# Performance work log

Hardware: AMD Instinct MI355X
Metric: run time of the kernel (lower is better)

Reference implementation:

```python
import jax, jax.numpy as jnp
import numpy as np

HIDDEN = 1024
BATCH = 4
SEQ = 4096
KQ = 4096  # number of query positions ('k' in the docstring)


def setup_inputs() -> dict:
    key = jax.random.key(0)
    ks = jax.random.split(key, 9)
    s = 1.0 / np.sqrt(HIDDEN)
    return {
        "queries": jax.random.normal(ks[0], (BATCH, KQ, HIDDEN), jnp.float32),
        "keys": jax.random.normal(ks[1], (BATCH, SEQ, HIDDEN), jnp.float32),
        "values": jax.random.normal(ks[2], (BATCH, SEQ, HIDDEN), jnp.float32),
        # nn.Linear params: y = x @ W.T + b
        "Wq": jax.random.normal(ks[3], (HIDDEN, HIDDEN), jnp.float32) * s,
        "bq": jax.random.normal(ks[4], (HIDDEN,), jnp.float32) * s,
        "Wk": jax.random.normal(ks[5], (HIDDEN, HIDDEN), jnp.float32) * s,
        "bk": jax.random.normal(ks[6], (HIDDEN,), jnp.float32) * s,
        "Wv": jax.random.normal(ks[7], (HIDDEN, HIDDEN), jnp.float32) * s,
        "bv": jax.random.normal(ks[8], (HIDDEN,), jnp.float32) * s,
    }


def reference(queries, keys, values, Wq, bq, Wk, bk, Wv, bv):
    hidden = keys.shape[-1]
    scaling = jax.lax.rsqrt(jnp.float32(hidden))
    q = jnp.einsum("bkh,oh->bko", queries, Wq) + bq  # [B, Kq, H]
    k = jnp.einsum("bsh,oh->bso", keys, Wk) + bk      # [B, S, H]
    v = jnp.einsum("bsh,oh->bso", values, Wv) + bv    # [B, S, H]
    # scores[b, s, kq] = k[b, s, :] . q[b, kq, :]
    scores = jnp.einsum("bsh,bkh->bsk", k, q) * scaling  # [B, S, Kq]
    # softmax over dim 1 (the seq_len / keys axis), as in nn.Softmax(dim=1)
    attention_weights = jax.nn.softmax(scores, axis=1)
    # context = attn^T @ v -> [B, Kq, H]
    context = jnp.einsum("bsk,bsh->bkh", attention_weights, v)
    return context, attention_weights
```

## Files before the change

### kernel.cpp

```cpp
#include <hip/hip_runtime.h>
#include <math.h>

#define HIDDEN 1024
#define NBATCH 4
#define SEQ    4096
#define NKQ    4096

typedef unsigned short us;
typedef __attribute__((ext_vector_type(8))) short short8;
typedef __attribute__((ext_vector_type(4))) float f32x4;

__device__ __forceinline__ us f2b(float f) {
    unsigned u = __float_as_uint(f);
    return (us)((u + 0x7fffu + ((u >> 16) & 1u)) >> 16);
}

__device__ __forceinline__ void glds16(const void* g, void* l) {
    __builtin_amdgcn_global_load_lds(
        (const __attribute__((address_space(1))) unsigned*)g,
        (__attribute__((address_space(3))) unsigned*)l, 16, 0, 0);
}

template <bool A_IS_F32, bool HAS_BIAS, bool OUT_BF16, bool SWZ>
__global__ __launch_bounds__(256) void gemm_nt(
    const void* __restrict__ Av, const us* __restrict__ B,
    const float* __restrict__ bias, void* __restrict__ Cv,
    int M, int N, int K, long sA, long sB, long sC, float scale)
{
    __shared__ us As[128 * 32];
    __shared__ us Bs[128 * 32];

    int bxi = blockIdx.x, byi = blockIdx.y, bzi = blockIdx.z;
    if (SWZ) {
        const int gx = gridDim.x, gy = gridDim.y;
        const int n  = gx * gy * gridDim.z;
        int lid = bxi + gx * (byi + gy * bzi);
        int nl  = (lid & 7) * (n >> 3) + (lid >> 3);
        bxi = nl % gx;
        nl /= gx;
        byi = nl % gy;
        bzi = nl / gy;
    }

    const int tid = threadIdx.x;
    const int bm = byi * 128;
    const int bn = bxi * 128;
    const int lane = tid & 63;
    const int wv   = tid >> 6;
    const int wm = (wv >> 1) * 64;
    const int wn = (wv & 1) * 64;
    const int fm = lane & 15;
    const int q8 = (lane >> 4) * 8;

    const us* Bg = B + (long)bzi * sB + (long)(bn + (tid >> 2)) * K + (tid & 3) * 8;
    us* BsT = &Bs[tid * 8];

    const us*    Agb = nullptr;
    const float* Agf = nullptr;
    us* AsTb = nullptr;
    us* AsTf = nullptr;
    if (A_IS_F32) {
        Agf  = (const float*)Av + (long)bzi * sA + (long)(bm + (tid >> 3)) * K + (tid & 7) * 4;
        AsTf = &As[(tid >> 3) * 32 + (tid & 7) * 4];
    } else {
        Agb  = (const us*)Av + (long)bzi * sA + (long)(bm + (tid >> 2)) * K + (tid & 3) * 8;
        AsTb = &As[tid * 8];
    }

    f32x4 acc[4][4];
#pragma unroll
    for (int i = 0; i < 4; i++)
#pragma unroll
        for (int j = 0; j < 4; j++)
            acc[i][j] = (f32x4){0.f, 0.f, 0.f, 0.f};

    for (int kt = 0; kt < K; kt += 32) {
        float4 fa[4];
        if (A_IS_F32) {
#pragma unroll
            for (int e = 0; e < 4; e++)
                fa[e] = *(const float4*)(Agf + (long)(32 * e) * K + kt);
        }
        __syncthreads();
        glds16(Bg + kt, BsT);
        glds16(Bg + kt + (long)64 * K, BsT + 2048);
        if (A_IS_F32) {
#pragma unroll
            for (int e = 0; e < 4; e++) {
                ushort4 h;
                h.x = f2b(fa[e].x); h.y = f2b(fa[e].y);
                h.z = f2b(fa[e].z); h.w = f2b(fa[e].w);
                *(ushort4*)(AsTf + 1024 * e) = h;
            }
        } else {
            glds16(Agb + kt, AsTb);
            glds16(Agb + kt + (long)64 * K, AsTb + 2048);
        }
        __syncthreads();

        short8 af[4], bf[4];
#pragma unroll
        for (int mi = 0; mi < 4; mi++)
            af[mi] = *(const short8*)&As[(wm + mi * 16 + fm) * 32 + q8];
#pragma unroll
        for (int ni = 0; ni < 4; ni++)
            bf[ni] = *(const short8*)&Bs[(wn + ni * 16 + fm) * 32 + q8];
#pragma unroll
        for (int mi = 0; mi < 4; mi++)
#pragma unroll
            for (int ni = 0; ni < 4; ni++)
                acc[mi][ni] = __builtin_amdgcn_mfma_f32_16x16x32_bf16(
                    af[mi], bf[ni], acc[mi][ni], 0, 0, 0);
    }

    const int er4 = (lane >> 4) * 4;
#pragma unroll
    for (int ni = 0; ni < 4; ni++) {
        const int col = bn + wn + ni * 16 + fm;
        const float bv = HAS_BIAS ? bias[col] : 0.0f;
#pragma unroll
        for (int mi = 0; mi < 4; mi++) {
#pragma unroll
            for (int r = 0; r < 4; r++) {
                const int row = bm + wm + mi * 16 + er4 + r;
                const float v = acc[mi][ni][r] * scale + bv;
                const long idx = (long)bzi * sC + (long)row * N + col;
                if (OUT_BF16) ((us*)Cv)[idx] = f2b(v);
                else          ((float*)Cv)[idx] = v;
            }
        }
    }
}

__global__ __launch_bounds__(256) void f2b_kernel(const float* __restrict__ in,
                                                  us* __restrict__ out, int n)
{
    const int i = (blockIdx.x * 256 + threadIdx.x) * 4;
    if (i < n) {
        const float4 f = *(const float4*)&in[i];
        ushort4 h;
        h.x = f2b(f.x); h.y = f2b(f.y); h.z = f2b(f.z); h.w = f2b(f.w);
        *(ushort4*)&out[i] = h;
    }
}

__global__ __launch_bounds__(256) void transpose_b_kernel(const us* __restrict__ in,
                                                          us* __restrict__ out)
{
    __shared__ us tile[64][72];
    const int t = threadIdx.x;
    const long ib = (long)blockIdx.z * SEQ * HIDDEN;
    const long ob = (long)blockIdx.z * (long)HIDDEN * SEQ;
    const int s0 = blockIdx.y * 64, h0 = blockIdx.x * 64;
    const int r = t >> 3, c = (t & 7) * 8;
#pragma unroll
    for (int e = 0; e < 2; e++) {
        const int rr = r + 32 * e;
        const uint4 v = *(const uint4*)&in[ib + (long)(s0 + rr) * HIDDEN + h0 + c];
        us* dst = &tile[rr][c];
        ((uint*)dst)[0] = v.x; ((uint*)dst)[1] = v.y;
        ((uint*)dst)[2] = v.z; ((uint*)dst)[3] = v.w;
    }
    __syncthreads();
#pragma unroll
    for (int e = 0; e < 2; e++) {
        const int rr = r + 32 * e;
        us vals[8];
#pragma unroll
        for (int j = 0; j < 8; j++) vals[j] = tile[c + j][rr];
        *(uint4*)&out[ob + (long)(h0 + rr) * SEQ + s0 + c] = *(uint4*)vals;
    }
}

__global__ __launch_bounds__(256) void softmax_rows_kernel(float* __restrict__ a,
                                                           us* __restrict__ ab)
{
    const long roff = ((long)blockIdx.y * NKQ + blockIdx.x) * SEQ;
    float* row = a + roff;
    us* rowb = ab + roff;
    const int t = threadIdx.x;
    const int lane = t & 63, wv = t >> 6;
    __shared__ float red[8];

    float4 x[4];
    float m = -INFINITY;
#pragma unroll
    for (int e = 0; e < 4; e++) {
        x[e] = *(const float4*)&row[t * 4 + 1024 * e];
        m = fmaxf(m, fmaxf(fmaxf(x[e].x, x[e].y), fmaxf(x[e].z, x[e].w)));
    }
#pragma unroll
    for (int o = 32; o; o >>= 1) m = fmaxf(m, __shfl_xor(m, o));
    if (lane == 0) red[wv] = m;
    __syncthreads();
    m = fmaxf(fmaxf(red[0], red[1]), fmaxf(red[2], red[3]));

    float s = 0.f;
#pragma unroll
    for (int e = 0; e < 4; e++) {
        x[e].x = __expf(x[e].x - m); x[e].y = __expf(x[e].y - m);
        x[e].z = __expf(x[e].z - m); x[e].w = __expf(x[e].w - m);
        s += x[e].x + x[e].y + x[e].z + x[e].w;
    }
#pragma unroll
    for (int o = 32; o; o >>= 1) s += __shfl_xor(s, o);
    if (lane == 0) red[4 + wv] = s;
    __syncthreads();
    s = red[4] + red[5] + red[6] + red[7];

    const float inv = 1.0f / s;
#pragma unroll
    for (int e = 0; e < 4; e++) {
        x[e].x *= inv; x[e].y *= inv; x[e].z *= inv; x[e].w *= inv;
        *(float4*)&row[t * 4 + 1024 * e] = x[e];
        ushort4 h;
        h.x = f2b(x[e].x); h.y = f2b(x[e].y);
        h.z = f2b(x[e].z); h.w = f2b(x[e].w);
        *(ushort4*)&rowb[t * 4 + 1024 * e] = h;
    }
}

__global__ __launch_bounds__(256) void transpose_f32_ip_kernel(float* __restrict__ a)
{
    const int ti = blockIdx.y, tj = blockIdx.x;
    if (tj < ti) return;
    float* base = a + (long)blockIdx.z * NKQ * SEQ;
    __shared__ float ta[64][65];
    __shared__ float tb[64][65];
    const int t = threadIdx.x, r = t >> 4, c = (t & 15) * 4;
    const bool diag = (ti == tj);
#pragma unroll
    for (int e = 0; e < 4; e++) {
        const int rr = r + 16 * e;
        const float4 va = *(const float4*)&base[(long)(ti * 64 + rr) * 4096 + tj * 64 + c];
        ta[rr][c] = va.x; ta[rr][c + 1] = va.y; ta[rr][c + 2] = va.z; ta[rr][c + 3] = va.w;
        if (!diag) {
            const float4 vb = *(const float4*)&base[(long)(tj * 64 + rr) * 4096 + ti * 64 + c];
            tb[rr][c] = vb.x; tb[rr][c + 1] = vb.y; tb[rr][c + 2] = vb.z; tb[rr][c + 3] = vb.w;
        }
    }
    __syncthreads();
#pragma unroll
    for (int e = 0; e < 4; e++) {
        const int rr = r + 16 * e;
        float4 w;
        w.x = ta[c][rr]; w.y = ta[c + 1][rr]; w.z = ta[c + 2][rr]; w.w = ta[c + 3][rr];
        *(float4*)&base[(long)(tj * 64 + rr) * 4096 + ti * 64 + c] = w;
        if (!diag) {
            float4 u;
            u.x = tb[c][rr]; u.y = tb[c + 1][rr]; u.z = tb[c + 2][rr]; u.w = tb[c + 3][rr];
            *(float4*)&base[(long)(ti * 64 + rr) * 4096 + tj * 64 + c] = u;
        }
    }
}

extern "C" void kernel_launch(void* const* d_in, const int* in_sizes, int n_in,
                              void* d_out, int out_size, void* d_ws, size_t ws_size,
                              hipStream_t stream)
{
    const float* queries = (const float*)d_in[0];
    const float* keys    = (const float*)d_in[1];
    const float* values  = (const float*)d_in[2];
    const float* Wq = (const float*)d_in[3]; const float* bq = (const float*)d_in[4];
    const float* Wk = (const float*)d_in[5]; const float* bk = (const float*)d_in[6];
    const float* Wv = (const float*)d_in[7]; const float* bv = (const float*)d_in[8];

    float* ctx  = (float*)d_out;
    float* attn = ctx + (long)NBATCH * NKQ * HIDDEN;

    char* ws = (char*)d_ws;
    us* vT_b = (us*)(ws);
    us* q_b  = (us*)(ws + (size_t)32  * 1024 * 1024);
    us* k_b  = (us*)(ws + (size_t)64  * 1024 * 1024);
    us* v_b  = (us*)(ws + (size_t)96  * 1024 * 1024);
    us* Wqb  = (us*)(ws + (size_t)128 * 1024 * 1024);
    us* Wkb  = Wqb + (size_t)HIDDEN * HIDDEN;
    us* Wvb  = Wkb + (size_t)HIDDEN * HIDDEN;
    us* attn_b = (us*)(ws + (size_t)32 * 1024 * 1024);

    const dim3 blk(256);
    const int nW = HIDDEN * HIDDEN;

    f2b_kernel<<<dim3(nW / 1024), blk, 0, stream>>>(Wq, Wqb, nW);
    f2b_kernel<<<dim3(nW / 1024), blk, 0, stream>>>(Wk, Wkb, nW);
    f2b_kernel<<<dim3(nW / 1024), blk, 0, stream>>>(Wv, Wvb, nW);

    gemm_nt<true, true, true, false><<<dim3(HIDDEN / 128, (NBATCH * NKQ) / 128, 1), blk, 0, stream>>>(
        queries, Wqb, bq, q_b, NBATCH * NKQ, HIDDEN, HIDDEN, 0, 0, 0, 1.0f);
    gemm_nt<true, true, true, false><<<dim3(HIDDEN / 128, (NBATCH * SEQ) / 128, 1), blk, 0, stream>>>(
        keys, Wkb, bk, k_b, NBATCH * SEQ, HIDDEN, HIDDEN, 0, 0, 0, 1.0f);
    gemm_nt<true, true, true, false><<<dim3(HIDDEN / 128, (NBATCH * SEQ) / 128, 1), blk, 0, stream>>>(
        values, Wvb, bv, v_b, NBATCH * SEQ, HIDDEN, HIDDEN, 0, 0, 0, 1.0f);

    transpose_b_kernel<<<dim3(HIDDEN / 64, SEQ / 64, NBATCH), blk, 0, stream>>>(v_b, vT_b);

    gemm_nt<false, false, false, false><<<dim3(SEQ / 128, NKQ / 128, NBATCH), blk, 0, stream>>>(
        q_b, k_b, nullptr, attn, NKQ, SEQ, HIDDEN,
        (long)NKQ * HIDDEN, (long)SEQ * HIDDEN, (long)NKQ * SEQ, 0.03125f);

    softmax_rows_kernel<<<dim3(NKQ, NBATCH), blk, 0, stream>>>(attn, attn_b);

    gemm_nt<false, false, false, true><<<dim3(HIDDEN / 128, NKQ / 128, NBATCH), blk, 0, stream>>>(
        attn_b, vT_b, nullptr, ctx, NKQ, HIDDEN, SEQ,
        (long)NKQ * SEQ, (long)HIDDEN * SEQ, (long)NKQ * HIDDEN, 1.0f);

    transpose_f32_ip_kernel<<<dim3(64, 64, NBATCH), blk, 0, stream>>>(attn);
}
```

Measured before the change: 1.435 ms.

## Add 256x256 double-buffered bf16 GEMM kernel for attention score and context matmuls

Adds a new 512-thread GEMM kernel with 256x256 output tiles and a K-step of 64. It double-buffers LDS through direct global-to-LDS loads, uses XOR-swizzled shared memory and raises wave priority around the MFMA blocks. The scores and context batched GEMMs switch to this kernel, and the projection GEMMs turn on block-index swizzling for L2 locality. Larger tiles cut global and LDS traffic per flop and overlap loads with compute, at the cost of heavy register use, 128 KB of LDS per block, and fewer blocks for the context GEMM grid (4x16x4).

After: 1.285 ms. -10.4%, faster.

```diff
diff --git a/kernel.cpp b/kernel.cpp
--- a/kernel.cpp
+++ b/kernel.cpp
@@ -19,6 +19,123 @@
     __builtin_amdgcn_global_load_lds(
         (const __attribute__((address_space(1))) unsigned*)g,
         (__attribute__((address_space(3))) unsigned*)l, 16, 0, 0);
+}
+
+__global__ __launch_bounds__(512, 2) void gemm_nt_256(
+    const us* __restrict__ A, const us* __restrict__ B, float* __restrict__ C,
+    int M, int N, int K, long sA, long sB, long sC, float scale)
+{
+    __shared__ us As[2][256 * 64];
+    __shared__ us Bs[2][256 * 64];
+
+    int bxi = blockIdx.x, byi = blockIdx.y, bzi = blockIdx.z;
+    {
+        const int gx = gridDim.x, gy = gridDim.y;
+        const int n  = gx * gy * gridDim.z;
+        int lid = bxi + gx * (byi + gy * bzi);
+        int nl  = (lid & 7) * (n >> 3) + (lid >> 3);
+        bxi = nl % gx;  nl /= gx;
+        byi = nl % gy;  bzi = nl / gy;
+    }
+
+    const int tid  = threadIdx.x;
+    const int lane = tid & 63;
+    const int wv   = tid >> 6;
+    const int wr   = wv >> 2;
+    const int wc   = wv & 3;
+    const int fm   = lane & 15;
+    const int l16  = lane >> 4;
+    const int bm   = byi * 256;
+    const int bn   = bxi * 256;
+
+    const int rA  = tid >> 3;
+    const int gsw = (tid & 7) ^ (rA & 7);
+    const us* Ag = A + (long)bzi * sA + (long)(bm + rA) * K + gsw * 8;
+    const us* Bg = B + (long)bzi * sB + (long)(bn + rA) * K + gsw * 8;
+    us* AsT0 = &As[0][tid * 8];  us* BsT0 = &Bs[0][tid * 8];
+    us* AsT1 = &As[1][tid * 8];  us* BsT1 = &Bs[1][tid * 8];
+
+    f32x4 acc[8][4];
+#pragma unroll
+    for (int i = 0; i < 8; i++)
+#pragma unroll
+        for (int j = 0; j < 4; j++)
+            acc[i][j] = (f32x4){0.f, 0.f, 0.f, 0.f};
+
+#pragma unroll
+    for (int j = 0; j < 4; j++) {
+        glds16(Ag + (long)(j * 64) * K, AsT0 + j * 4096);
+        glds16(Bg + (long)(j * 64) * K, BsT0 + j * 4096);
+    }
+    asm volatile("s_waitcnt vmcnt(0)" ::: "memory");
+    __builtin_amdgcn_s_barrier();
+
+    const int xr = (fm & 7) * 8;
+
+    int cur = 0;
+    for (int kt = 0; kt < K; kt += 64) {
+        const int ktn = kt + 64;
+        const bool pf = ktn < K;
+        const us* Asb = As[cur];
+        const us* Bsb = Bs[cur];
+        us* AsTn = cur ? AsT0 : AsT1;
+        us* BsTn = cur ? BsT0 : BsT1;
+
+#pragma unroll
+        for (int q = 0; q < 4; q++) {
+            const int mh = q & 1, nh = q >> 1;
+            short8 a[4][2], b[2][2];
+#pragma unroll
+            for (int m = 0; m < 4; m++) {
+                const int arow = wr * 128 + (mh * 4 + m) * 16 + fm;
+#pragma unroll
+                for (int kk = 0; kk < 2; kk++)
+                    a[m][kk] = *(const short8*)&Asb[arow * 64 + (((kk * 4 + l16) * 8) ^ xr)];
+            }
+#pragma unroll
+            for (int n = 0; n < 2; n++) {
+                const int brow = wc * 64 + (nh * 2 + n) * 16 + fm;
+#pragma unroll
+                for (int kk = 0; kk < 2; kk++)
+                    b[n][kk] = *(const short8*)&Bsb[brow * 64 + (((kk * 4 + l16) * 8) ^ xr)];
+            }
+            if (pf) {
+                glds16(Ag + (long)(q * 64) * K + ktn, AsTn + q * 4096);
+                glds16(Bg + (long)(q * 64) * K + ktn, BsTn + q * 4096);
+            }
+            __builtin_amdgcn_s_barrier();
+            __builtin_amdgcn_s_setprio(1);
+#pragma unroll
+            for (int m = 0; m < 4; m++)
+#pragma unroll
+                for (int n = 0; n < 2; n++)
+#pragma unroll
+                    for (int kk = 0; kk < 2; kk++)
+                        acc[mh * 4 + m][nh * 2 + n] = __builtin_amdgcn_mfma_f32_16x16x32_bf16(
+                            a[m][kk], b[n][kk], acc[mh * 4 + m][nh * 2 + n], 0, 0, 0);
+            __builtin_amdgcn_s_setprio(0);
+            if (q < 3) {
+                __builtin_amdgcn_s_barrier();
+            } else {
+                asm volatile("s_waitcnt vmcnt(0)" ::: "memory");
+                __builtin_amdgcn_s_barrier();
+            }
+        }
+        cur ^= 1;
+    }
+
+    const int er4 = l16 * 4;
+#pragma unroll
+    for (int ni = 0; ni < 4; ni++) {
+        const int col = bn + wc * 64 + ni * 16 + fm;
+#pragma unroll
+        for (int mi = 0; mi < 8; mi++) {
+            const int row = bm + wr * 128 + mi * 16 + er4;
+#pragma unroll
+            for (int r = 0; r < 4; r++)
+                C[(long)bzi * sC + (long)(row + r) * N + col] = acc[mi][ni][r] * scale;
+        }
+    }
 }
 
 template <bool A_IS_F32, bool HAS_BIAS, bool OUT_BF16, bool SWZ>
@@ -279,29 +396,30 @@
     us* attn_b = (us*)(ws + (size_t)32 * 1024 * 1024);
 
     const dim3 blk(256);
+    const dim3 blk2(512);
     const int nW = HIDDEN * HIDDEN;
 
     f2b_kernel<<<dim3(nW / 1024), blk, 0, stream>>>(Wq, Wqb, nW);
     f2b_kernel<<<dim3(nW / 1024), blk, 0, stream>>>(Wk, Wkb, nW);
     f2b_kernel<<<dim3(nW / 1024), blk, 0, stream>>>(Wv, Wvb, nW);
 
-    gemm_nt<true, true, true, false><<<dim3(HIDDEN / 128, (NBATCH * NKQ) / 128, 1), blk, 0, stream>>>(
+    gemm_nt<true, true, true, true><<<dim3(HIDDEN / 128, (NBATCH * NKQ) / 128, 1), blk, 0, stream>>>(
         queries, Wqb, bq, q_b, NBATCH * NKQ, HIDDEN, HIDDEN, 0, 0, 0, 1.0f);
-    gemm_nt<true, true, true, false><<<dim3(HIDDEN / 128, (NBATCH * SEQ) / 128, 1), blk, 0, stream>>>(
+    gemm_nt<true, true, true, true><<<dim3(HIDDEN / 128, (NBATCH * SEQ) / 128, 1), blk, 0, stream>>>(
         keys, Wkb, bk, k_b, NBATCH * SEQ, HIDDEN, HIDDEN, 0, 0, 0, 1.0f);
-    gemm_nt<true, true, true, false><<<dim3(HIDDEN / 128, (NBATCH * SEQ) / 128, 1), blk, 0, stream>>>(
+    gemm_nt<true, true, true, true><<<dim3(HIDDEN / 128, (NBATCH * SEQ) / 128, 1), blk, 0, stream>>>(
         values, Wvb, bv, v_b, NBATCH * SEQ, HIDDEN, HIDDEN, 0, 0, 0, 1.0f);
 
     transpose_b_kernel<<<dim3(HIDDEN / 64, SEQ / 64, NBATCH), blk, 0, stream>>>(v_b, vT_b);
 
-    gemm_nt<false, false, false, false><<<dim3(SEQ / 128, NKQ / 128, NBATCH), blk, 0, stream>>>(
-        q_b, k_b, nullptr, attn, NKQ, SEQ, HIDDEN,
+    gemm_nt_256<<<dim3(SEQ / 256, NKQ / 256, NBATCH), blk2, 0, stream>>>(
+        q_b, k_b, attn, NKQ, SEQ, HIDDEN,
         (long)NKQ * HIDDEN, (long)SEQ * HIDDEN, (long)NKQ * SEQ, 0.03125f);
 
     softmax_rows_kernel<<<dim3(NKQ, NBATCH), blk, 0, stream>>>(attn, attn_b);
 
-    gemm_nt<false, false, false, true><<<dim3(HIDDEN / 128, NKQ / 128, NBATCH), blk, 0, stream>>>(
-        attn_b, vT_b, nullptr, ctx, NKQ, HIDDEN, SEQ,
+    gemm_nt_256<<<dim3(HIDDEN / 256, NKQ / 256, NBATCH), blk2, 0, stream>>>(
+        attn_b, vT_b, ctx, NKQ, HIDDEN, SEQ,
         (long)NKQ * SEQ, (long)HIDDEN * SEQ, (long)NKQ * HIDDEN, 1.0f);
 
     transpose_f32_ip_kernel<<<dim3(64, 64, NBATCH), blk, 0, stream>>>(attn);
```
